# Performance work log

Measured on AMD Instinct MI355X. Metric: run time of the kernel, lower is better.

The kernel has to match this reference:

```python
import jax, jax.numpy as jnp
import numpy as np

B, S, D, H, T = 64, 512, 768, 384, 22  # batch, seq, bert dim, lstm hidden, tagset+2


def setup_inputs() -> dict:
    key = jax.random.key(0)
    ks = jax.random.split(key, 14)
    hidden_states = jax.random.normal(ks[0], (B, S, D), jnp.float32)
    # strictly increasing wordpiece start offsets, -1 padded (per-sample variable length)
    nw = np.array([S // 2 - (b % 16) * 4 for b in range(B)])  # number of valid start ids
    sid = -np.ones((B, S), np.int64)
    msk = np.zeros((B, S), np.int64)
    for b in range(B):
        sid[b, : nw[b]] = 1 + 2 * np.arange(nw[b])  # max = 2*nw-1 <= S-1
        msk[b, : nw[b] + 1] = 1  # word-level mask: nw+1 words incl. CLS slot
    start_ids = jnp.asarray(sid)
    masks = jnp.asarray(msk)
    sc = 0.05
    h0 = jax.random.normal(ks[1], (2, B, H), jnp.float32)
    c0 = jax.random.normal(ks[2], (2, B, H), jnp.float32)
    W_ih_f = jax.random.normal(ks[3], (4 * H, D), jnp.float32) * sc
    W_hh_f = jax.random.normal(ks[4], (4 * H, H), jnp.float32) * sc
    b_ih_f = jax.random.normal(ks[5], (4 * H,), jnp.float32) * sc
    b_hh_f = jax.random.normal(ks[6], (4 * H,), jnp.float32) * sc
    W_ih_b = jax.random.normal(ks[7], (4 * H, D), jnp.float32) * sc
    W_hh_b = jax.random.normal(ks[8], (4 * H, H), jnp.float32) * sc
    b_ih_b = jax.random.normal(ks[9], (4 * H,), jnp.float32) * sc
    b_hh_b = jax.random.normal(ks[10], (4 * H,), jnp.float32) * sc
    W_lin = jax.random.normal(ks[11], (T, 2 * H), jnp.float32) * sc
    b_lin = jax.random.normal(ks[12], (T,), jnp.float32) * sc
    return {"hidden_states": hidden_states, "h0": h0, "c0": c0,
            "W_ih_f": W_ih_f, "W_hh_f": W_hh_f, "b_ih_f": b_ih_f, "b_hh_f": b_hh_f,
            "W_ih_b": W_ih_b, "W_hh_b": W_hh_b, "b_ih_b": b_ih_b, "b_hh_b": b_hh_b,
            "W_lin": W_lin, "b_lin": b_lin, "start_ids": start_ids, "masks": masks}


def _lstm_dir(x, h0, c0, Wih, Whh, bih, bhh, reverse):
    # x: [B,S,D]; torch gate order i,f,g,o
    xg = jnp.einsum('bsd,gd->bsg', x, Wih) + bih + bhh  # [B,S,4H]
    xs = jnp.swapaxes(xg, 0, 1)  # [S,B,4H]
    if reverse:
        xs = xs[::-1]

    def step(carry, xt):
        h, c = carry
        g = xt + h @ Whh.T
        i, f, gg, o = jnp.split(g, 4, axis=-1)
        c = jax.nn.sigmoid(f) * c + jax.nn.sigmoid(i) * jnp.tanh(gg)
        h = jax.nn.sigmoid(o) * jnp.tanh(c)
        return (h, c), h

    _, hs = jax.lax.scan(step, (h0, c0), xs)
    if reverse:
        hs = hs[::-1]
    return jnp.swapaxes(hs, 0, 1)  # [B,S,H]


def _align(hidden_states, start_ids, masks):
    # word t embedding: t==0 -> token 0 (CLS); 1<=t<n -> token start_ids[t]-1
    # (last wordpiece of word t); t==n -> token start_ids[n-1]; else zero-pad.
    Bb, Ss, _ = hidden_states.shape
    t = jnp.arange(Ss)[None, :]
    valid = start_ids >= 0
    n = valid.sum(-1)  # [B] number of valid start ids
    last_sid = jnp.take_along_axis(start_ids, (n - 1)[:, None], axis=1)  # [B,1]
    idx = jnp.where(t == 0, 0,
          jnp.where(t < n[:, None], start_ids - 1,
          jnp.where(t == n[:, None], last_sid, 0)))
    idx = jnp.clip(idx, 0, Ss - 1)
    gathered = jnp.take_along_axis(hidden_states, idx[:, :, None], axis=1)
    sent_len = masks.sum(-1)  # word-level lengths (second loop in torch code)
    keep = (t < sent_len[:, None])[:, :, None]
    return jnp.where(keep, gathered, 0.0)


def reference(hidden_states, h0, c0, W_ih_f, W_hh_f, b_ih_f, b_hh_f,
              W_ih_b, W_hh_b, b_ih_b, b_hh_b, W_lin, b_lin, start_ids, masks):
    embeds = _align(hidden_states, start_ids, masks)  # q=1,k=0 => wordpiece-only
    hf = _lstm_dir(embeds, h0[0], c0[0], W_ih_f, W_hh_f, b_ih_f, b_hh_f, False)
    hb = _lstm_dir(embeds, h0[1], c0[1], W_ih_b, W_hh_b, b_ih_b, b_hh_b, True)
    lstm_out = jnp.concatenate([hf, hb], axis=-1)  # [B,S,2H]
    # dropout1 is identity in eval mode
    feats = lstm_out @ W_lin.T + b_lin  # [B,S,T]
    return feats
```

## Files before the change

kernel.cpp:

```cpp
#include <hip/hip_runtime.h>

typedef unsigned short u16;
typedef unsigned int u32;
typedef unsigned long long u64;

typedef short bf16x8 __attribute__((ext_vector_type(8)));
typedef float f32x4 __attribute__((ext_vector_type(4)));

#define NB 64
#define NS 512
#define ND 768
#define NH 384
#define NT_OUT 22
#define S2 272
#define NG 1536
#define MGEMM (NB*S2)

__device__ __forceinline__ u16 f2b(float f) {
    u32 u = __float_as_uint(f);
    u32 r = (u + 0x7fffu + ((u >> 16) & 1u)) >> 16;
    return (u16)r;
}
__device__ __forceinline__ float b2f(u16 s) { return __uint_as_float(((u32)s) << 16); }

__device__ __forceinline__ float sigm(float x) {
    return __builtin_amdgcn_rcpf(1.f + __expf(-x));
}
__device__ __forceinline__ float tanh_(float x) {
    return 1.f - 2.f * __builtin_amdgcn_rcpf(1.f + __expf(2.f * x));
}

__device__ __forceinline__ void gl_lds16(const void* g, void* l) {
    __builtin_amdgcn_global_load_lds(
        (const __attribute__((address_space(1))) unsigned int*)g,
        (__attribute__((address_space(3))) unsigned int*)l, 16, 0, 0);
}

__global__ void k_prep(const float* __restrict__ hidden, const int* __restrict__ start_ids,
                       const int* __restrict__ masks, u16* __restrict__ embeds) {
    int b = blockIdx.x >> 2;
    int quarter = blockIdx.x & 3;
    int tid = threadIdx.x;
    __shared__ int red[256];
    int cn = 0, cm = 0;
    for (int s = tid; s < NS; s += 256) {
        cn += (start_ids[b * NS + s] >= 0) ? 1 : 0;
        cm += (masks[b * NS + s] != 0) ? 1 : 0;
    }
    red[tid] = cn + (cm << 16);
    __syncthreads();
    #pragma unroll
    for (int off = 128; off > 0; off >>= 1) {
        if (tid < off) red[tid] += red[tid + off];
        __syncthreads();
    }
    int n = red[0] & 0xffff;
    int slen = red[0] >> 16;
    n = min(max(n, 1), NS);
    int last = start_ids[b * NS + n - 1];
    for (int t = quarter * 68; t < quarter * 68 + 68; ++t) {
        int idx;
        if (t == 0) idx = 0;
        else if (t < n) idx = start_ids[b * NS + t] - 1;
        else if (t == n) idx = last;
        else idx = 0;
        idx = min(max(idx, 0), NS - 1);
        bool keep = t < slen;
        const float* src = hidden + ((size_t)b * NS + idx) * ND;
        u16* dst = embeds + ((size_t)b * S2 + t) * ND;
        if (tid < 192) {
            float4 v = keep ? *(const float4*)(src + tid * 4) : make_float4(0.f, 0.f, 0.f, 0.f);
            union { u16 u[4]; uint2 q; } pk;
            pk.u[0] = f2b(v.x); pk.u[1] = f2b(v.y); pk.u[2] = f2b(v.z); pk.u[3] = f2b(v.w);
            *(uint2*)(dst + tid * 4) = pk.q;
        }
    }
}

__global__ void k_weights(const float* __restrict__ wf, const float* __restrict__ wb,
                          const float* __restrict__ bihf, const float* __restrict__ bhhf,
                          const float* __restrict__ bihb, const float* __restrict__ bhhb,
                          const float* __restrict__ h0,
                          u16* __restrict__ wihcat, float* __restrict__ biascat,
                          u16* __restrict__ h0buf) {
    int i0 = blockIdx.x * blockDim.x + threadIdx.x;
    int NTH = gridDim.x * blockDim.x;
    for (size_t i = i0; i < (size_t)2 * NG * ND; i += NTH) {
        size_t nrow = i / ND, k = i - nrow * ND;
        float v = (nrow < NG) ? wf[nrow * ND + k] : wb[(nrow - NG) * ND + k];
        wihcat[i] = f2b(v);
    }
    for (int i = i0; i < 2 * NG; i += NTH)
        biascat[i] = (i < NG) ? bihf[i] + bhhf[i] : bihb[i - NG] + bhhb[i - NG];
    for (int i = i0; i < 2 * NB * NH; i += NTH) h0buf[i] = f2b(h0[i]);
}

__global__ void k_packwhh(const float* __restrict__ whhf, const float* __restrict__ whhb,
                          u16* __restrict__ pack) {
    int ft = blockIdx.x * 256 + threadIdx.x;
    if (ft >= 2 * 4 * 4 * 6 * 12 * 64) return;
    int lane = ft & 63;
    int grp = ft >> 6;
    int ks = grp % 12; grp /= 12;
    int nt = grp % 6;  grp /= 6;
    int w  = grp & 3;  grp >>= 2;
    int qc = grp & 3;
    int d  = grp >> 2;
    const float* W = d ? whhb : whhf;
    int col = w * NH + qc * 96 + nt * 16 + (lane & 15);
    int k0 = ks * 32 + (lane >> 4) * 8;
    u16* dst = pack + (size_t)ft * 8;
    #pragma unroll
    for (int e = 0; e < 8; e++) dst[e] = f2b(W[(size_t)col * NH + k0 + e]);
}

__launch_bounds__(256, 2)
__global__ void k_gemm(const u16* __restrict__ A, const u16* __restrict__ Bw,
                       const float* __restrict__ biascat, u16* __restrict__ xg) {
    __shared__ u16 As[128 * 32];
    __shared__ u16 Bs[128 * 32];
    int tid = threadIdx.x;
    int lane = tid & 63, wid = tid >> 6;
    int l15 = lane & 15, q4 = lane >> 4;
    int bn = blockIdx.x;
    int bm = blockIdx.y;
    int wm = (wid >> 1) * 64, wn = (wid & 1) * 64;
    f32x4 acc[4][4] = {};
    for (int k0 = 0; k0 < ND; k0 += 32) {
        #pragma unroll
        for (int j = 0; j < 2; j++) {
            int fl = tid + j * 256;
            int row = fl >> 2, cb = fl & 3;
            const u16* ga = A + (size_t)(bm * 128 + row) * ND + k0 + cb * 8;
            gl_lds16(ga, &As[(size_t)(wid * 64 + j * 256) * 8]);
            const u16* gb = Bw + (size_t)(bn * 128 + row) * ND + k0 + cb * 8;
            gl_lds16(gb, &Bs[(size_t)(wid * 64 + j * 256) * 8]);
        }
        __syncthreads();
        bf16x8 af[4], bf[4];
        #pragma unroll
        for (int mt = 0; mt < 4; mt++)
            af[mt] = *(const bf16x8*)&As[(wm + mt * 16 + l15) * 32 + q4 * 8];
        #pragma unroll
        for (int nt = 0; nt < 4; nt++)
            bf[nt] = *(const bf16x8*)&Bs[(wn + nt * 16 + l15) * 32 + q4 * 8];
        #pragma unroll
        for (int mt = 0; mt < 4; mt++)
            #pragma unroll
            for (int nt = 0; nt < 4; nt++)
                acc[mt][nt] = __builtin_amdgcn_mfma_f32_16x16x32_bf16(af[mt], bf[nt], acc[mt][nt], 0, 0, 0);
        __syncthreads();
    }
    #pragma unroll
    for (int nt = 0; nt < 4; nt++) {
        int gn = bn * 128 + wn + nt * 16 + l15;
        int d = gn >= NG ? 1 : 0;
        int col = gn - d * NG;
        float bias = biascat[gn];
        #pragma unroll
        for (int mt = 0; mt < 4; mt++) {
            #pragma unroll
            for (int r = 0; r < 4; r++) {
                int m = bm * 128 + wm + mt * 16 + q4 * 4 + r;
                int b = m / S2, t = m - b * S2;
                float v = acc[mt][nt][r] + bias;
                xg[((size_t)(d * NB + b) * S2 + t) * NG + col] = f2b(v);
            }
        }
    }
}

__launch_bounds__(256, 1)
__global__ void k_recur(const u16* __restrict__ whhpack, const u16* __restrict__ xg,
                        const float* __restrict__ biascat, const u16* __restrict__ h0buf,
                        const float* __restrict__ c0, u16* __restrict__ hout,
                        int* __restrict__ flags) {
    int blk = blockIdx.x;
    int qc = blk >> 3;
    int cl = blk & 7;
    int d = cl >> 2;
    int g = cl & 3;
    int tid = threadIdx.x, lane = tid & 63, w = tid >> 6;
    int q4 = lane >> 4, l15 = lane & 15;

    __shared__ float preact[4][16 * 96];

    bf16x8 bfr[6][12];
    #pragma unroll
    for (int nt = 0; nt < 6; nt++)
        #pragma unroll
        for (int ks = 0; ks < 12; ks++)
            bfr[nt][ks] = *(const bf16x8*)(whhpack +
                ((size_t)((((d * 4 + qc) * 4 + w) * 6 + nt) * 12 + ks) * 64 + lane) * 8);

    int bb = tid / 12;
    int j0 = (tid % 12) * 8;
    float cre[8];
    if (tid < 192) {
        const float* cp = c0 + (size_t)(d * NB + g * 16 + bb) * NH + qc * 96 + j0;
        #pragma unroll
        for (int e = 0; e < 8; e++) cre[e] = cp[e];
    }
    float biasreg[6];
    #pragma unroll
    for (int nt = 0; nt < 6; nt++)
        biasreg[nt] = biascat[d * NG + w * NH + qc * 96 + nt * 16 + l15];

    int* flagp = flags + cl * NS;
    const u16* hd = hout + (size_t)d * NB * NS * NH;
    const u16* xgd = xg + (size_t)d * NB * S2 * NG;

    float ci[6][4];
    auto preload = [&](int it2) {
        int s2 = d ? (NS - 1 - it2) : it2;
        if (s2 < S2) {
            const u16* xrow = xgd + ((size_t)(g * 16) * S2 + s2) * NG + w * NH + qc * 96 + l15;
            #pragma unroll
            for (int nt = 0; nt < 6; nt++)
                #pragma unroll
                for (int r = 0; r < 4; r++)
                    ci[nt][r] = b2f(xrow[(size_t)(q4 * 4 + r) * S2 * NG + nt * 16]);
        } else {
            #pragma unroll
            for (int nt = 0; nt < 6; nt++)
                #pragma unroll
                for (int r = 0; r < 4; r++) ci[nt][r] = biasreg[nt];
        }
    };
    preload(0);

    int dep = 0;
    #pragma unroll 1
    for (int it = 0; it < NS; ++it) {
        int s = d ? (NS - 1 - it) : it;
        int tprev = d ? (s + 1) : (s - 1);

        bf16x8 af[12];
        if (it == 0) {
            const u16* hp = h0buf + (size_t)(d * NB + g * 16) * NH;
            #pragma unroll
            for (int ks = 0; ks < 12; ks++)
                af[ks] = *(const bf16x8*)(hp + (size_t)l15 * NH + ks * 32 + q4 * 8);
        } else {
            const u64* hp = (const u64*)(hd + ((size_t)(g * 16) * NS + tprev) * NH) + dep;
            #pragma unroll
            for (int ks = 0; ks < 12; ks++) {
                union { u64 q[2]; bf16x8 v; } u;
                const u64* p = hp + ((size_t)l15 * NS * NH + (size_t)ks * 32 + q4 * 8) / 4;
                u.q[0] = __hip_atomic_load(p,     __ATOMIC_RELAXED, __HIP_MEMORY_SCOPE_AGENT);
                u.q[1] = __hip_atomic_load(p + 1, __ATOMIC_RELAXED, __HIP_MEMORY_SCOPE_AGENT);
                af[ks] = u.v;
            }
        }

        f32x4 acc[6];
        #pragma unroll
        for (int nt = 0; nt < 6; nt++) {
            acc[nt][0] = ci[nt][0]; acc[nt][1] = ci[nt][1];
            acc[nt][2] = ci[nt][2]; acc[nt][3] = ci[nt][3];
        }
        #pragma unroll
        for (int ks = 0; ks < 12; ks++)
            #pragma unroll
            for (int nt = 0; nt < 6; nt++)
                acc[nt] = __builtin_amdgcn_mfma_f32_16x16x32_bf16(af[ks], bfr[nt][ks], acc[nt], 0, 0, 0);

        #pragma unroll
        for (int nt = 0; nt < 6; nt++)
            #pragma unroll
            for (int r = 0; r < 4; r++)
                preact[w][(q4 * 4 + r) * 96 + nt * 16 + l15] = acc[nt][r];
        __syncthreads();

        if (tid < 192) {
            int idx = bb * 96 + j0;
            u16* ho = hout + (((size_t)(d * NB + g * 16 + bb)) * NS + s) * NH + qc * 96 + j0;
            union { u16 u[8]; u64 q[2]; } pk;
            #pragma unroll
            for (int e = 0; e < 8; e++) {
                float gi = preact[0][idx + e], gf = preact[1][idx + e];
                float gg = preact[2][idx + e], go = preact[3][idx + e];
                float c = cre[e];
                float cn = sigm(gf) * c + sigm(gi) * tanh_(gg);
                float hn = sigm(go) * tanh_(cn);
                cre[e] = cn;
                pk.u[e] = f2b(hn);
            }
            __hip_atomic_store((u64*)ho,     pk.q[0], __ATOMIC_RELAXED, __HIP_MEMORY_SCOPE_AGENT);
            __hip_atomic_store((u64*)ho + 1, pk.q[1], __ATOMIC_RELAXED, __HIP_MEMORY_SCOPE_AGENT);
        }
        __syncthreads();

        if (tid == 0)
            __hip_atomic_fetch_add(&flagp[it], 1, __ATOMIC_RELAXED, __HIP_MEMORY_SCOPE_AGENT);

        if (it == NS - 1) break;

        preload(it + 1);

        int fv = 4;
        if (lane == 0) {
            while ((fv = __hip_atomic_load(&flagp[it], __ATOMIC_RELAXED, __HIP_MEMORY_SCOPE_AGENT)) < 4)
                __builtin_amdgcn_s_sleep(1);
        }
        fv = __shfl(fv, 0);
        dep = fv - 4;
    }
}

__global__ void k_final(const u16* __restrict__ hout, const float* __restrict__ wlin,
                        const float* __restrict__ blin, float* __restrict__ out) {
    int r = blockIdx.x * 256 + threadIdx.x;
    int b = r >> 9, t = r & 511;
    const u16* hf = hout + ((size_t)b * NS + t) * NH;
    const u16* hb = hout + ((size_t)(NB + b) * NS + t) * NH;
    float acc[NT_OUT];
    #pragma unroll
    for (int tt = 0; tt < NT_OUT; tt++) acc[tt] = blin[tt];
    #pragma unroll 1
    for (int half = 0; half < 2; half++) {
        const u16* hp = half ? hb : hf;
        #pragma unroll 1
        for (int k8 = 0; k8 < NH / 8; k8++) {
            uint4 pk = *(const uint4*)(hp + k8 * 8);
            float x[8];
            x[0] = __uint_as_float(pk.x << 16); x[1] = __uint_as_float(pk.x & 0xffff0000u);
            x[2] = __uint_as_float(pk.y << 16); x[3] = __uint_as_float(pk.y & 0xffff0000u);
            x[4] = __uint_as_float(pk.z << 16); x[5] = __uint_as_float(pk.z & 0xffff0000u);
            x[6] = __uint_as_float(pk.w << 16); x[7] = __uint_as_float(pk.w & 0xffff0000u);
            int kk = half * NH + k8 * 8;
            #pragma unroll
            for (int e = 0; e < 8; e++)
                #pragma unroll
                for (int tt = 0; tt < NT_OUT; tt++)
                    acc[tt] += x[e] * wlin[tt * (2 * NH) + kk + e];
        }
    }
    float* op = out + (size_t)r * NT_OUT;
    #pragma unroll
    for (int tt = 0; tt < NT_OUT; tt++) op[tt] = acc[tt];
}

extern "C" void kernel_launch(void* const* d_in, const int* in_sizes, int n_in,
                              void* d_out, int out_size, void* d_ws, size_t ws_size,
                              hipStream_t stream) {
    const float* hidden = (const float*)d_in[0];
    const float* h0     = (const float*)d_in[1];
    const float* c0     = (const float*)d_in[2];
    const float* Wihf   = (const float*)d_in[3];
    const float* Whhf   = (const float*)d_in[4];
    const float* bihf   = (const float*)d_in[5];
    const float* bhhf   = (const float*)d_in[6];
    const float* Wihb   = (const float*)d_in[7];
    const float* Whhb   = (const float*)d_in[8];
    const float* bihb   = (const float*)d_in[9];
    const float* bhhb   = (const float*)d_in[10];
    const float* Wlin   = (const float*)d_in[11];
    const float* blin   = (const float*)d_in[12];
    const int* start_ids = (const int*)d_in[13];
    const int* masks     = (const int*)d_in[14];
    float* out = (float*)d_out;

    char* ws = (char*)d_ws;
    size_t off = 0;
    auto alloc = [&](size_t bytes) { void* p = ws + off; off += (bytes + 255) & ~(size_t)255; return p; };
    u16* embeds   = (u16*)alloc((size_t)MGEMM * ND * 2);
    u16* wihcat   = (u16*)alloc((size_t)2 * NG * ND * 2);
    float* biascat = (float*)alloc((size_t)2 * NG * 4);
    u16* whhpack  = (u16*)alloc((size_t)2 * NG * NH * 2);
    u16* h0buf    = (u16*)alloc((size_t)2 * NB * NH * 2);
    u16* xg       = (u16*)alloc((size_t)2 * NB * S2 * NG * 2);
    u16* hout     = (u16*)alloc((size_t)2 * NB * NS * NH * 2);
    int* flags    = (int*)alloc((size_t)8 * NS * 4);

    (void)hipMemsetAsync(flags, 0, (size_t)8 * NS * 4, stream);
    k_prep<<<256, 256, 0, stream>>>(hidden, start_ids, masks, embeds);
    k_weights<<<512, 256, 0, stream>>>(Wihf, Wihb, bihf, bhhf, bihb, bhhb, h0,
                                       wihcat, biascat, h0buf);
    k_packwhh<<<576, 256, 0, stream>>>(Whhf, Whhb, whhpack);
    dim3 ggrid(2 * NG / 128, MGEMM / 128);
    k_gemm<<<ggrid, 256, 0, stream>>>(embeds, wihcat, biascat, xg);
    k_recur<<<32, 256, 0, stream>>>(whhpack, xg, biascat, h0buf, c0, hout, flags);
    k_final<<<128, 256, 0, stream>>>(hout, Wlin, blin, out);
}
```

Baseline: 3.034 ms.

## Interleave both LSTM directions per block and store h in MFMA-fragment layout

The recurrent kernel is repartitioned. Each of the 32 blocks now owns a 48-column slice for both directions, instead of one direction with a 96-column slice. While one direction's cross-block flag wait is outstanding, the other direction's MFMA work can run, hiding some of the sync latency. The hidden state is written per timestep in a layout that matches the A-fragment, so the next step reads it with contiguous coalesced loads instead of strided rows. The final projection is rewritten to read this new layout and to stage W_lin in LDS. Each block now holds twice the weight registers split across directions, and the flag threshold rises to 8 blocks, which adds synchronisation participants per step.

Result: slower. 11.35 ms (+273.9%).

```diff
diff --git a/kernel.cpp b/kernel.cpp
--- a/kernel.cpp
+++ b/kernel.cpp
@@ -15,6 +15,7 @@
 #define S2 272
 #define NG 1536
 #define MGEMM (NB*S2)
+#define HXS 6144
 
 __device__ __forceinline__ u16 f2b(float f) {
     u32 u = __float_as_uint(f);
@@ -98,20 +99,20 @@
 __global__ void k_packwhh(const float* __restrict__ whhf, const float* __restrict__ whhb,
                           u16* __restrict__ pack) {
     int ft = blockIdx.x * 256 + threadIdx.x;
-    if (ft >= 2 * 4 * 4 * 6 * 12 * 64) return;
+    if (ft >= 2 * 8 * 4 * 3 * 12 * 64) return;
     int lane = ft & 63;
     int grp = ft >> 6;
     int ks = grp % 12; grp /= 12;
-    int nt = grp % 6;  grp /= 6;
+    int nt = grp % 3;  grp /= 3;
     int w  = grp & 3;  grp >>= 2;
-    int qc = grp & 3;
-    int d  = grp >> 2;
+    int jc = grp & 7;
+    int d  = grp >> 3;
     const float* W = d ? whhb : whhf;
-    int col = w * NH + qc * 96 + nt * 16 + (lane & 15);
+    int row = w * NH + jc * 48 + nt * 16 + (lane & 15);
     int k0 = ks * 32 + (lane >> 4) * 8;
     u16* dst = pack + (size_t)ft * 8;
     #pragma unroll
-    for (int e = 0; e < 8; e++) dst[e] = f2b(W[(size_t)col * NH + k0 + e]);
+    for (int e = 0; e < 8; e++) dst[e] = f2b(W[(size_t)row * NH + k0 + e]);
 }
 
 __launch_bounds__(256, 2)
@@ -173,170 +174,179 @@
 __launch_bounds__(256, 1)
 __global__ void k_recur(const u16* __restrict__ whhpack, const u16* __restrict__ xg,
                         const float* __restrict__ biascat, const u16* __restrict__ h0buf,
-                        const float* __restrict__ c0, u16* __restrict__ hout,
+                        const float* __restrict__ c0, u16* __restrict__ hx,
                         int* __restrict__ flags) {
     int blk = blockIdx.x;
-    int qc = blk >> 3;
-    int cl = blk & 7;
-    int d = cl >> 2;
-    int g = cl & 3;
+    int jc = blk >> 2;
+    int g = blk & 3;
     int tid = threadIdx.x, lane = tid & 63, w = tid >> 6;
     int q4 = lane >> 4, l15 = lane & 15;
 
-    __shared__ float preact[4][16 * 96];
-
-    bf16x8 bfr[6][12];
-    #pragma unroll
-    for (int nt = 0; nt < 6; nt++)
-        #pragma unroll
-        for (int ks = 0; ks < 12; ks++)
-            bfr[nt][ks] = *(const bf16x8*)(whhpack +
-                ((size_t)((((d * 4 + qc) * 4 + w) * 6 + nt) * 12 + ks) * 64 + lane) * 8);
-
-    int bb = tid / 12;
-    int j0 = (tid % 12) * 8;
-    float cre[8];
-    if (tid < 192) {
-        const float* cp = c0 + (size_t)(d * NB + g * 16 + bb) * NH + qc * 96 + j0;
-        #pragma unroll
-        for (int e = 0; e < 8; e++) cre[e] = cp[e];
-    }
-    float biasreg[6];
-    #pragma unroll
-    for (int nt = 0; nt < 6; nt++)
-        biasreg[nt] = biascat[d * NG + w * NH + qc * 96 + nt * 16 + l15];
-
-    int* flagp = flags + cl * NS;
-    const u16* hd = hout + (size_t)d * NB * NS * NH;
-    const u16* xgd = xg + (size_t)d * NB * S2 * NG;
-
-    float ci[6][4];
-    auto preload = [&](int it2) {
+    __shared__ float preact[4][16][49];
+
+    bf16x8 bfr[2][3][12];
+    #pragma unroll
+    for (int d = 0; d < 2; d++)
+        #pragma unroll
+        for (int nt = 0; nt < 3; nt++)
+            #pragma unroll
+            for (int ks = 0; ks < 12; ks++)
+                bfr[d][nt][ks] = *(const bf16x8*)(whhpack +
+                    ((size_t)((((d * 8 + jc) * 4 + w) * 3 + nt) * 12 + ks) * 64 + lane) * 8);
+
+    int bb = tid / 6, jo = (tid % 6) * 8;
+    float cre[2][8];
+    if (tid < 96) {
+        #pragma unroll
+        for (int d = 0; d < 2; d++)
+            #pragma unroll
+            for (int e = 0; e < 8; e++)
+                cre[d][e] = c0[((size_t)(d * NB + g * 16 + bb)) * NH + jc * 48 + jo + e];
+    }
+    float biasreg[2][3];
+    #pragma unroll
+    for (int d = 0; d < 2; d++)
+        #pragma unroll
+        for (int nt = 0; nt < 3; nt++)
+            biasreg[d][nt] = biascat[d * NG + w * NH + jc * 48 + nt * 16 + l15];
+
+    float ci[2][3][4];
+    auto preload = [&](int d, int it2) {
         int s2 = d ? (NS - 1 - it2) : it2;
         if (s2 < S2) {
-            const u16* xrow = xgd + ((size_t)(g * 16) * S2 + s2) * NG + w * NH + qc * 96 + l15;
-            #pragma unroll
-            for (int nt = 0; nt < 6; nt++)
+            const u16* xrow = xg + ((size_t)(d * NB + g * 16) * S2 + s2) * NG
+                              + w * NH + jc * 48 + l15;
+            #pragma unroll
+            for (int nt = 0; nt < 3; nt++)
                 #pragma unroll
                 for (int r = 0; r < 4; r++)
-                    ci[nt][r] = b2f(xrow[(size_t)(q4 * 4 + r) * S2 * NG + nt * 16]);
+                    ci[d][nt][r] = b2f(xrow[(size_t)(q4 * 4 + r) * S2 * NG + nt * 16]);
         } else {
             #pragma unroll
-            for (int nt = 0; nt < 6; nt++)
-                #pragma unroll
-                for (int r = 0; r < 4; r++) ci[nt][r] = biasreg[nt];
+            for (int nt = 0; nt < 3; nt++)
+                #pragma unroll
+                for (int r = 0; r < 4; r++) ci[d][nt][r] = biasreg[d][nt];
         }
     };
-    preload(0);
-
-    int dep = 0;
+
+    bf16x8 af[2][12];
+    #pragma unroll
+    for (int d = 0; d < 2; d++)
+        #pragma unroll
+        for (int ks = 0; ks < 12; ks++)
+            af[d][ks] = *(const bf16x8*)(h0buf +
+                ((size_t)(d * NB + g * 16 + l15)) * NH + ks * 32 + q4 * 8);
+    preload(0, 0);
+    preload(1, 0);
+
+    int ggi16 = ((jc * 48 + jo) >> 3) * 16 + bb;
+
     #pragma unroll 1
     for (int it = 0; it < NS; ++it) {
-        int s = d ? (NS - 1 - it) : it;
-        int tprev = d ? (s + 1) : (s - 1);
-
-        bf16x8 af[12];
-        if (it == 0) {
-            const u16* hp = h0buf + (size_t)(d * NB + g * 16) * NH;
+        #pragma unroll 1
+        for (int d = 0; d < 2; d++) {
+            f32x4 acc[3];
+            #pragma unroll
+            for (int nt = 0; nt < 3; nt++) {
+                acc[nt][0] = ci[d][nt][0]; acc[nt][1] = ci[d][nt][1];
+                acc[nt][2] = ci[d][nt][2]; acc[nt][3] = ci[d][nt][3];
+            }
             #pragma unroll
             for (int ks = 0; ks < 12; ks++)
-                af[ks] = *(const bf16x8*)(hp + (size_t)l15 * NH + ks * 32 + q4 * 8);
-        } else {
-            const u64* hp = (const u64*)(hd + ((size_t)(g * 16) * NS + tprev) * NH) + dep;
+                #pragma unroll
+                for (int nt = 0; nt < 3; nt++)
+                    acc[nt] = __builtin_amdgcn_mfma_f32_16x16x32_bf16(af[d][ks], bfr[d][nt][ks], acc[nt], 0, 0, 0);
+
+            #pragma unroll
+            for (int nt = 0; nt < 3; nt++)
+                #pragma unroll
+                for (int r = 0; r < 4; r++)
+                    preact[w][q4 * 4 + r][nt * 16 + l15] = acc[nt][r];
+            __syncthreads();
+
+            if (tid < 96) {
+                union { u16 u[8]; u64 q[2]; } pk;
+                #pragma unroll
+                for (int e = 0; e < 8; e++) {
+                    float gi = preact[0][bb][jo + e], gf = preact[1][bb][jo + e];
+                    float gg = preact[2][bb][jo + e], go = preact[3][bb][jo + e];
+                    float c = cre[d][e];
+                    float cn = sigm(gf) * c + sigm(gi) * tanh_(gg);
+                    float hn = sigm(go) * tanh_(cn);
+                    cre[d][e] = cn;
+                    pk.u[e] = f2b(hn);
+                }
+                u64* hp = (u64*)(hx + ((size_t)((d * 4 + g) * NS + it)) * HXS
+                                 + (size_t)ggi16 * 8);
+                __hip_atomic_store(hp,     pk.q[0], __ATOMIC_RELAXED, __HIP_MEMORY_SCOPE_AGENT);
+                __hip_atomic_store(hp + 1, pk.q[1], __ATOMIC_RELAXED, __HIP_MEMORY_SCOPE_AGENT);
+            }
+            __syncthreads();
+
+            if (tid == 0)
+                __hip_atomic_fetch_add(&flags[(d * 4 + g) * NS + it], 1,
+                                       __ATOMIC_RELAXED, __HIP_MEMORY_SCOPE_AGENT);
+            if (it < NS - 1) preload(d, it + 1);
+        }
+
+        if (it == NS - 1) break;
+
+        #pragma unroll 1
+        for (int d = 0; d < 2; d++) {
+            int fv = 8;
+            if (lane == 0) {
+                while ((fv = __hip_atomic_load(&flags[(d * 4 + g) * NS + it],
+                        __ATOMIC_RELAXED, __HIP_MEMORY_SCOPE_AGENT)) < 8)
+                    __builtin_amdgcn_s_sleep(1);
+            }
+            fv = __shfl(fv, 0);
+            int dep = fv - 8;
+            const u64* hb = (const u64*)(hx + ((size_t)((d * 4 + g) * NS + it)) * HXS) + dep;
             #pragma unroll
             for (int ks = 0; ks < 12; ks++) {
                 union { u64 q[2]; bf16x8 v; } u;
-                const u64* p = hp + ((size_t)l15 * NS * NH + (size_t)ks * 32 + q4 * 8) / 4;
+                const u64* p = hb + (size_t)(ks * 64 + lane) * 2;
                 u.q[0] = __hip_atomic_load(p,     __ATOMIC_RELAXED, __HIP_MEMORY_SCOPE_AGENT);
                 u.q[1] = __hip_atomic_load(p + 1, __ATOMIC_RELAXED, __HIP_MEMORY_SCOPE_AGENT);
-                af[ks] = u.v;
-            }
-        }
-
-        f32x4 acc[6];
-        #pragma unroll
-        for (int nt = 0; nt < 6; nt++) {
-            acc[nt][0] = ci[nt][0]; acc[nt][1] = ci[nt][1];
-            acc[nt][2] = ci[nt][2]; acc[nt][3] = ci[nt][3];
-        }
-        #pragma unroll
-        for (int ks = 0; ks < 12; ks++)
-            #pragma unroll
-            for (int nt = 0; nt < 6; nt++)
-                acc[nt] = __builtin_amdgcn_mfma_f32_16x16x32_bf16(af[ks], bfr[nt][ks], acc[nt], 0, 0, 0);
-
-        #pragma unroll
-        for (int nt = 0; nt < 6; nt++)
-            #pragma unroll
-            for (int r = 0; r < 4; r++)
-                preact[w][(q4 * 4 + r) * 96 + nt * 16 + l15] = acc[nt][r];
-        __syncthreads();
-
-        if (tid < 192) {
-            int idx = bb * 96 + j0;
-            u16* ho = hout + (((size_t)(d * NB + g * 16 + bb)) * NS + s) * NH + qc * 96 + j0;
-            union { u16 u[8]; u64 q[2]; } pk;
-            #pragma unroll
-            for (int e = 0; e < 8; e++) {
-                float gi = preact[0][idx + e], gf = preact[1][idx + e];
-                float gg = preact[2][idx + e], go = preact[3][idx + e];
-                float c = cre[e];
-                float cn = sigm(gf) * c + sigm(gi) * tanh_(gg);
-                float hn = sigm(go) * tanh_(cn);
-                cre[e] = cn;
-                pk.u[e] = f2b(hn);
-            }
-            __hip_atomic_store((u64*)ho,     pk.q[0], __ATOMIC_RELAXED, __HIP_MEMORY_SCOPE_AGENT);
-            __hip_atomic_store((u64*)ho + 1, pk.q[1], __ATOMIC_RELAXED, __HIP_MEMORY_SCOPE_AGENT);
-        }
-        __syncthreads();
-
-        if (tid == 0)
-            __hip_atomic_fetch_add(&flagp[it], 1, __ATOMIC_RELAXED, __HIP_MEMORY_SCOPE_AGENT);
-
-        if (it == NS - 1) break;
-
-        preload(it + 1);
-
-        int fv = 4;
-        if (lane == 0) {
-            while ((fv = __hip_atomic_load(&flagp[it], __ATOMIC_RELAXED, __HIP_MEMORY_SCOPE_AGENT)) < 4)
-                __builtin_amdgcn_s_sleep(1);
-        }
-        fv = __shfl(fv, 0);
-        dep = fv - 4;
-    }
-}
-
-__global__ void k_final(const u16* __restrict__ hout, const float* __restrict__ wlin,
+                af[d][ks] = u.v;
+            }
+        }
+    }
+}
+
+__global__ void k_final(const u16* __restrict__ hx, const float* __restrict__ wlin,
                         const float* __restrict__ blin, float* __restrict__ out) {
-    int r = blockIdx.x * 256 + threadIdx.x;
-    int b = r >> 9, t = r & 511;
-    const u16* hf = hout + ((size_t)b * NS + t) * NH;
-    const u16* hb = hout + ((size_t)(NB + b) * NS + t) * NH;
+    __shared__ float wlds[NT_OUT * 2 * NH];
+    int tid = threadIdx.x;
+    for (int i = tid; i < NT_OUT * 2 * NH; i += 256) wlds[i] = wlin[i];
+    __syncthreads();
+    int b = blockIdx.x >> 1;
+    int t = (blockIdx.x & 1) * 256 + tid;
+    int g = b >> 4, m = b & 15;
     float acc[NT_OUT];
     #pragma unroll
     for (int tt = 0; tt < NT_OUT; tt++) acc[tt] = blin[tt];
     #pragma unroll 1
-    for (int half = 0; half < 2; half++) {
-        const u16* hp = half ? hb : hf;
+    for (int d = 0; d < 2; d++) {
+        int it = d ? (NS - 1 - t) : t;
+        const u16* hb = hx + ((size_t)((d * 4 + g) * NS + it)) * HXS;
         #pragma unroll 1
-        for (int k8 = 0; k8 < NH / 8; k8++) {
-            uint4 pk = *(const uint4*)(hp + k8 * 8);
+        for (int gi = 0; gi < 48; gi++) {
+            uint4 pk = *(const uint4*)(hb + ((size_t)gi * 16 + m) * 8);
             float x[8];
             x[0] = __uint_as_float(pk.x << 16); x[1] = __uint_as_float(pk.x & 0xffff0000u);
             x[2] = __uint_as_float(pk.y << 16); x[3] = __uint_as_float(pk.y & 0xffff0000u);
             x[4] = __uint_as_float(pk.z << 16); x[5] = __uint_as_float(pk.z & 0xffff0000u);
             x[6] = __uint_as_float(pk.w << 16); x[7] = __uint_as_float(pk.w & 0xffff0000u);
-            int kk = half * NH + k8 * 8;
+            int col = d * NH + gi * 8;
             #pragma unroll
             for (int e = 0; e < 8; e++)
                 #pragma unroll
                 for (int tt = 0; tt < NT_OUT; tt++)
-                    acc[tt] += x[e] * wlin[tt * (2 * NH) + kk + e];
-        }
-    }
-    float* op = out + (size_t)r * NT_OUT;
+                    acc[tt] += x[e] * wlds[tt * (2 * NH) + col + e];
+        }
+    }
+    float* op = out + ((size_t)b * NS + t) * NT_OUT;
     #pragma unroll
     for (int tt = 0; tt < NT_OUT; tt++) op[tt] = acc[tt];
 }
@@ -370,7 +380,7 @@
     u16* whhpack  = (u16*)alloc((size_t)2 * NG * NH * 2);
     u16* h0buf    = (u16*)alloc((size_t)2 * NB * NH * 2);
     u16* xg       = (u16*)alloc((size_t)2 * NB * S2 * NG * 2);
-    u16* hout     = (u16*)alloc((size_t)2 * NB * NS * NH * 2);
+    u16* hx       = (u16*)alloc((size_t)8 * NS * HXS * 2);
     int* flags    = (int*)alloc((size_t)8 * NS * 4);
 
     (void)hipMemsetAsync(flags, 0, (size_t)8 * NS * 4, stream);
@@ -380,6 +390,6 @@
     k_packwhh<<<576, 256, 0, stream>>>(Whhf, Whhb, whhpack);
     dim3 ggrid(2 * NG / 128, MGEMM / 128);
     k_gemm<<<ggrid, 256, 0, stream>>>(embeds, wihcat, biascat, xg);
-    k_recur<<<32, 256, 0, stream>>>(whhpack, xg, biascat, h0buf, c0, hout, flags);
-    k_final<<<128, 256, 0, stream>>>(hout, Wlin, blin, out);
-}
+    k_recur<<<32, 256, 0, stream>>>(whhpack, xg, biascat, h0buf, c0, hx, flags);
+    k_final<<<128, 256, 0, stream>>>(hx, Wlin, blin, out);
+}
```
